# Optimization experiments

Hardware: AMD Instinct MI355X
Metric: run time of the kernel (lower is better)

## Reference

```python
import jax, jax.numpy as jnp
import numpy as np

N_NODES = 50000


def _build_graph(edge_index):
    # Add self-loops (PyG GCNConv default) and compute symmetric normalization.
    n = N_NODES
    loops = jnp.arange(n, dtype=edge_index.dtype)
    src = jnp.concatenate([edge_index[0], loops])
    dst = jnp.concatenate([edge_index[1], loops])
    deg = jax.ops.segment_sum(jnp.ones_like(dst, dtype=jnp.float32), dst, num_segments=n)
    dinv = jax.lax.rsqrt(jnp.maximum(deg, 1e-12))
    norm = dinv[src] * dinv[dst]  # [E+N]
    return src, dst, norm


def _gcn_layer(h, src, dst, norm, W, b):
    # transform-then-propagate: out[dst] += norm * (h @ W)[src]
    h = h @ W  # [N, D_out]
    msg = h[src] * norm[:, None]  # [E+N, D_out]
    agg = jax.ops.segment_sum(msg, dst, num_segments=N_NODES)
    return agg + b


def setup_inputs() -> dict:
    key = jax.random.key(0)
    ks = jax.random.split(key, 8)
    in_dim, hid, out = 128, 64, 32
    n_edges = 800000
    x = jax.random.normal(ks[0], (N_NODES, in_dim), dtype=jnp.float32)
    edge_index = jax.random.randint(ks[1], (2, n_edges), 0, N_NODES, dtype=jnp.int32)
    W1 = jax.random.normal(ks[2], (in_dim, hid), dtype=jnp.float32) / np.sqrt(in_dim)
    b1 = jnp.zeros((hid,), jnp.float32)
    W2 = jax.random.normal(ks[3], (hid, out), dtype=jnp.float32) / np.sqrt(hid)
    b2 = jnp.zeros((out,), jnp.float32)
    attn_w = jax.random.normal(ks[4], (out, 1), dtype=jnp.float32) / np.sqrt(out)
    attn_b = jnp.zeros((1,), jnp.float32)
    return {"x": x, "edge_index": edge_index, "W1": W1, "b1": b1,
            "W2": W2, "b2": b2, "attn_w": attn_w, "attn_b": attn_b}


def reference(x, edge_index, W1, b1, W2, b2, attn_w, attn_b):
    src, dst, norm = _build_graph(edge_index)
    h = jax.nn.relu(_gcn_layer(x, src, dst, norm, W1, b1))
    h = jax.nn.relu(_gcn_layer(h, src, dst, norm, W2, b2))
    attn = jax.nn.sigmoid(h @ attn_w + attn_b)  # [N, 1]
    return h * attn
```

## Files before the change

kernel.cpp:

```cpp
#include <hip/hip_runtime.h>
#include <math.h>

#define N_NODES 50000
#define SLICE_SZ 6250

__global__ void count_kernel(const int* __restrict__ dst, int E, int* __restrict__ counts) {
    int i = blockIdx.x * blockDim.x + threadIdx.x;
    if (i < E) atomicAdd(&counts[dst[i]], 1);
}

__global__ void scan_block_kernel(const int* __restrict__ in, int n,
                                  int* __restrict__ outEx, int* __restrict__ blocksum) {
    __shared__ int s[256];
    int t = threadIdx.x, i = blockIdx.x * 256 + t;
    int v = (i < n) ? in[i] : 0;
    s[t] = v;
    __syncthreads();
    for (int off = 1; off < 256; off <<= 1) {
        int x = (t >= off) ? s[t - off] : 0;
        __syncthreads();
        s[t] += x;
        __syncthreads();
    }
    if (i < n) outEx[i] = s[t] - v;
    if (t == 255 && blocksum) blocksum[blockIdx.x] = s[255];
}

__global__ void finalize_kernel(const int* __restrict__ counts, const int* __restrict__ blocksum,
                                int n, int E, int* __restrict__ row_ptr,
                                int* __restrict__ cursor, float* __restrict__ dinv) {
    int i = blockIdx.x * blockDim.x + threadIdx.x;
    if (i < n) {
        int rp = row_ptr[i] + blocksum[i >> 8];
        row_ptr[i] = rp;
        cursor[i]  = rp;
        dinv[i] = rsqrtf((float)(counts[i] + 1));
        if (i == 0) row_ptr[n] = E;
    }
}

__global__ void fill_sliced_kernel(const int* __restrict__ src, const int* __restrict__ dst,
                                   int E, int* __restrict__ cursor,
                                   const float* __restrict__ dinv, int2* __restrict__ edges) {
    const int slice = blockIdx.x & 7;
    const int chunk = blockIdx.x >> 3;
    const int CS = (E + 255) / 256;
    int lo = chunk * CS;
    int hi = min(E, lo + CS);
    for (int i = lo + threadIdx.x; i < hi; i += 256) {
        int d = dst[i];
        if (d / SLICE_SZ == slice) {
            int s = src[i];
            int p = atomicAdd(&cursor[d], 1);
            edges[p] = make_int2(s, __float_as_int(dinv[s] * dinv[d]));
        }
    }
}

template<int DIN, int DOUT, int BM, int KC>
__global__ __launch_bounds__(256, 2) void gemm_kernel(const float* __restrict__ A,
                                                      const float* __restrict__ W,
                                                      float* __restrict__ C, int n) {
    constexpr int NCG = DOUT / 4;
    constexpr int NRG = BM / 4;
    static_assert(NCG * NRG == 256, "thread mapping");
    constexpr int KG = KC / 4;
    constexpr int RSTEP = 256 / KG;
    __shared__ __align__(16) float ws[DIN * DOUT];
    __shared__ __align__(16) float xs[KC][BM + 4];
    const int t = threadIdx.x;
    for (int i = 4 * t; i < DIN * DOUT; i += 1024)
        *(float4*)&ws[i] = *(const float4*)&W[i];
    const int rowbase = blockIdx.x * BM;
    const int r0 = (t / NCG) * 4;
    const int c0 = (t % NCG) * 4;
    const int lk = (t % KG) * 4;
    const int lr = t / KG;
    float acc[4][4] = {};
    for (int kc = 0; kc < DIN; kc += KC) {
        __syncthreads();
        #pragma unroll
        for (int r = lr; r < BM; r += RSTEP) {
            int row = rowbase + r;
            if (row >= n) row = n - 1;
            float4 v = *(const float4*)&A[(size_t)row * DIN + kc + lk];
            xs[lk + 0][r] = v.x; xs[lk + 1][r] = v.y;
            xs[lk + 2][r] = v.z; xs[lk + 3][r] = v.w;
        }
        __syncthreads();
        #pragma unroll 8
        for (int k = 0; k < KC; ++k) {
            float ar[4], wr[4];
            *(float4*)ar = *(const float4*)&xs[k][r0];
            *(float4*)wr = *(const float4*)&ws[(kc + k) * DOUT + c0];
            #pragma unroll
            for (int i = 0; i < 4; ++i)
                #pragma unroll
                for (int j = 0; j < 4; ++j)
                    acc[i][j] += ar[i] * wr[j];
        }
    }
    #pragma unroll
    for (int i = 0; i < 4; ++i) {
        int row = rowbase + r0 + i;
        if (row < n) {
            float4 v = make_float4(acc[i][0], acc[i][1], acc[i][2], acc[i][3]);
            *(float4*)&C[(size_t)row * DOUT + c0] = v;
        }
    }
}

__global__ __launch_bounds__(256) void gather64_fuse_kernel(
        const float* __restrict__ XW, const int* __restrict__ row_ptr,
        const int2* __restrict__ edges, const float* __restrict__ dinv,
        const float* __restrict__ b1, const float* __restrict__ W2,
        float* __restrict__ out, int n) {
    __shared__ __align__(16) float ws2[64 * 32];
    const int t = threadIdx.x;
    for (int i = 4 * t; i < 64 * 32; i += 1024)
        *(float4*)&ws2[i] = *(const float4*)&W2[i];
    __syncthreads();
    int gid = blockIdx.x * blockDim.x + t;
    int node = gid >> 6;
    int f = t & 63;
    if (node < n) {
        float dv = dinv[node];
        float acc = dv * dv * XW[(size_t)node * 64 + f];
        int e = row_ptr[node], end = row_ptr[node + 1];
        for (; e + 8 <= end; e += 8) {
            int2 p0 = edges[e+0], p1 = edges[e+1], p2 = edges[e+2], p3 = edges[e+3];
            int2 p4 = edges[e+4], p5 = edges[e+5], p6 = edges[e+6], p7 = edges[e+7];
            float v0 = XW[(size_t)p0.x * 64 + f], v1 = XW[(size_t)p1.x * 64 + f];
            float v2 = XW[(size_t)p2.x * 64 + f], v3 = XW[(size_t)p3.x * 64 + f];
            float v4 = XW[(size_t)p4.x * 64 + f], v5 = XW[(size_t)p5.x * 64 + f];
            float v6 = XW[(size_t)p6.x * 64 + f], v7 = XW[(size_t)p7.x * 64 + f];
            acc += __int_as_float(p0.y) * v0; acc += __int_as_float(p1.y) * v1;
            acc += __int_as_float(p2.y) * v2; acc += __int_as_float(p3.y) * v3;
            acc += __int_as_float(p4.y) * v4; acc += __int_as_float(p5.y) * v5;
            acc += __int_as_float(p6.y) * v6; acc += __int_as_float(p7.y) * v7;
        }
        if (e + 4 <= end) {
            int2 p0 = edges[e+0], p1 = edges[e+1], p2 = edges[e+2], p3 = edges[e+3];
            float v0 = XW[(size_t)p0.x * 64 + f], v1 = XW[(size_t)p1.x * 64 + f];
            float v2 = XW[(size_t)p2.x * 64 + f], v3 = XW[(size_t)p3.x * 64 + f];
            acc += __int_as_float(p0.y) * v0; acc += __int_as_float(p1.y) * v1;
            acc += __int_as_float(p2.y) * v2; acc += __int_as_float(p3.y) * v3;
            e += 4;
        }
        for (; e < end; ++e) {
            int2 p = edges[e];
            acc += __int_as_float(p.y) * XW[(size_t)p.x * 64 + f];
        }
        float h = fmaxf(acc + b1[f], 0.f);
        int j = f & 31, half = f >> 5;
        int fbase = half << 5;
        float y = 0.f;
        #pragma unroll
        for (int k = 0; k < 32; ++k) {
            float hf = __shfl(h, fbase + k, 64);
            y += hf * ws2[(fbase + k) * 32 + j];
        }
        y += __shfl_xor(y, 32, 64);
        if (half == 0) out[(size_t)node * 32 + j] = y;
    }
}

__global__ __launch_bounds__(256) void gather32_final_kernel(
        const float* __restrict__ XW, const int* __restrict__ row_ptr,
        const int2* __restrict__ edges, const float* __restrict__ dinv,
        const float* __restrict__ bias, const float* __restrict__ aw,
        const float* __restrict__ ab, float* __restrict__ out, int n) {
    int gid = blockIdx.x * blockDim.x + threadIdx.x;
    int node = gid >> 6;
    int lane = threadIdx.x & 63;
    int f = lane & 31, half = lane >> 5;
    if (node >= n) return;
    float acc = 0.f;
    if (half == 0) {
        float dv = dinv[node];
        acc = dv * dv * XW[(size_t)node * 32 + f];
    }
    int end = row_ptr[node + 1];
    int e = row_ptr[node] + half;
    for (; e + 6 < end; e += 8) {
        int2 p0 = edges[e+0], p1 = edges[e+2], p2 = edges[e+4], p3 = edges[e+6];
        float v0 = XW[(size_t)p0.x * 32 + f], v1 = XW[(size_t)p1.x * 32 + f];
        float v2 = XW[(size_t)p2.x * 32 + f], v3 = XW[(size_t)p3.x * 32 + f];
        acc += __int_as_float(p0.y) * v0; acc += __int_as_float(p1.y) * v1;
        acc += __int_as_float(p2.y) * v2; acc += __int_as_float(p3.y) * v3;
    }
    for (; e < end; e += 2) {
        int2 p = edges[e];
        acc += __int_as_float(p.y) * XW[(size_t)p.x * 32 + f];
    }
    acc += __shfl_xor(acc, 32, 64);
    float h = fmaxf(acc + bias[f], 0.f);
    float sca = h * aw[f];
    #pragma unroll
    for (int m = 16; m >= 1; m >>= 1) sca += __shfl_xor(sca, m, 64);
    float attn = 1.f / (1.f + __expf(-(sca + ab[0])));
    if (half == 0) out[(size_t)node * 32 + f] = h * attn;
}

extern "C" void kernel_launch(void* const* d_in, const int* in_sizes, int n_in,
                              void* d_out, int out_size, void* d_ws, size_t ws_size,
                              hipStream_t stream) {
    const float* x  = (const float*)d_in[0];
    const int*   ei = (const int*)d_in[1];
    const float* W1 = (const float*)d_in[2];
    const float* b1 = (const float*)d_in[3];
    const float* W2 = (const float*)d_in[4];
    const float* b2 = (const float*)d_in[5];
    const float* aw = (const float*)d_in[6];
    const float* ab = (const float*)d_in[7];
    float* out = (float*)d_out;

    const int n = N_NODES;
    const int E = in_sizes[1] / 2;
    const int* src = ei;
    const int* dst = ei + E;

    char* w = (char*)d_ws;
    auto alloc = [&](size_t bytes) { char* p = w; w += (bytes + 255) & ~(size_t)255; return p; };
    int*   counts   = (int*)  alloc((size_t)n * 4);
    int*   row_ptr  = (int*)  alloc((size_t)(n + 1) * 4);
    int*   cursor   = (int*)  alloc((size_t)n * 4);
    int*   blocksum = (int*)  alloc(1024);
    float* dinv     = (float*)alloc((size_t)n * 4);
    int2*  edges    = (int2*) alloc((size_t)E * 8);
    float* bufA     = (float*)alloc((size_t)n * 64 * 4);
    float* bufB     = (float*)alloc((size_t)n * 32 * 4);

    const int nb = (n + 255) / 256;

    hipMemsetAsync(counts, 0, (size_t)n * 4, stream);
    count_kernel<<<(E + 255) / 256, 256, 0, stream>>>(dst, E, counts);
    scan_block_kernel<<<nb, 256, 0, stream>>>(counts, n, row_ptr, blocksum);
    scan_block_kernel<<<1, 256, 0, stream>>>(blocksum, nb, blocksum, nullptr);
    finalize_kernel<<<nb, 256, 0, stream>>>(counts, blocksum, n, E, row_ptr, cursor, dinv);
    fill_sliced_kernel<<<256 * 8, 256, 0, stream>>>(src, dst, E, cursor, dinv, edges);

    gemm_kernel<128, 64, 64, 32><<<(n + 63) / 64, 256, 0, stream>>>(x, W1, bufA, n);
    gather64_fuse_kernel<<<((size_t)n * 64 + 255) / 256, 256, 0, stream>>>(
        bufA, row_ptr, edges, dinv, b1, W2, bufB, n);
    gather32_final_kernel<<<((size_t)n * 64 + 255) / 256, 256, 0, stream>>>(
        bufB, row_ptr, edges, dinv, b2, aw, ab, out, n);
}
```

Before: 263.3 us.

## Precompute edge ranks in count pass and vectorize gathers with float4 multi-way lanes

The count kernel now records each edge's atomic rank, so the fill kernel computes CSR positions as row_ptr plus rank with no second atomic pass. The fill kernel also reads dst as int4. Both gather kernels switch from one-feature-per-lane scalar loads to float4 loads, with several lanes ('ways') splitting each node's edges and combining through shuffle reductions. The layer-2 matvec uses a padded, permuted shared-memory copy of W2. This cuts atomics and memory transactions, at the cost of an extra E-sized rank buffer and more shuffle work.

```diff
diff --git a/kernel.cpp b/kernel.cpp
--- a/kernel.cpp
+++ b/kernel.cpp
@@ -4,9 +4,14 @@
 #define N_NODES 50000
 #define SLICE_SZ 6250
 
-__global__ void count_kernel(const int* __restrict__ dst, int E, int* __restrict__ counts) {
+__device__ __forceinline__ void fma4(float4& a, float w, const float4& v) {
+    a.x += w * v.x; a.y += w * v.y; a.z += w * v.z; a.w += w * v.w;
+}
+
+__global__ void count_kernel(const int* __restrict__ dst, int E,
+                             int* __restrict__ counts, int* __restrict__ rank) {
     int i = blockIdx.x * blockDim.x + threadIdx.x;
-    if (i < E) atomicAdd(&counts[dst[i]], 1);
+    if (i < E) rank[i] = atomicAdd(&counts[dst[i]], 1);
 }
 
 __global__ void scan_block_kernel(const int* __restrict__ in, int n,
@@ -28,30 +33,44 @@
 
 __global__ void finalize_kernel(const int* __restrict__ counts, const int* __restrict__ blocksum,
                                 int n, int E, int* __restrict__ row_ptr,
-                                int* __restrict__ cursor, float* __restrict__ dinv) {
+                                float* __restrict__ dinv) {
     int i = blockIdx.x * blockDim.x + threadIdx.x;
     if (i < n) {
-        int rp = row_ptr[i] + blocksum[i >> 8];
-        row_ptr[i] = rp;
-        cursor[i]  = rp;
+        row_ptr[i] += blocksum[i >> 8];
         dinv[i] = rsqrtf((float)(counts[i] + 1));
         if (i == 0) row_ptr[n] = E;
     }
 }
 
-__global__ void fill_sliced_kernel(const int* __restrict__ src, const int* __restrict__ dst,
-                                   int E, int* __restrict__ cursor,
-                                   const float* __restrict__ dinv, int2* __restrict__ edges) {
+__global__ void fill2_kernel(const int* __restrict__ src, const int* __restrict__ dst,
+                             const int* __restrict__ rank, int E,
+                             const int* __restrict__ row_ptr, const float* __restrict__ dinv,
+                             int2* __restrict__ edges) {
     const int slice = blockIdx.x & 7;
     const int chunk = blockIdx.x >> 3;
-    const int CS = (E + 255) / 256;
-    int lo = chunk * CS;
-    int hi = min(E, lo + CS);
-    for (int i = lo + threadIdx.x; i < hi; i += 256) {
+    const int CS = (((E + 255) >> 8) + 3) & ~3;
+    const int lo = chunk * CS;
+    const int hi = min(E, lo + CS);
+    const int slo = slice * SLICE_SZ, shi = slo + SLICE_SZ;
+    if (lo >= E) return;
+    const int quad_end = lo + ((hi - lo) & ~3);
+    for (int i = lo + threadIdx.x * 4; i + 3 < quad_end + 4 && i + 3 < hi + 4 && i < quad_end; i += 1024) {
+        int4 d4 = *(const int4*)&dst[i];
+        #pragma unroll
+        for (int k = 0; k < 4; ++k) {
+            int d = (&d4.x)[k];
+            if (d >= slo && d < shi) {
+                int s = src[i + k];
+                int p = row_ptr[d] + rank[i + k];
+                edges[p] = make_int2(s, __float_as_int(dinv[s] * dinv[d]));
+            }
+        }
+    }
+    for (int i = quad_end + threadIdx.x; i < hi; i += 256) {
         int d = dst[i];
-        if (d / SLICE_SZ == slice) {
+        if (d >= slo && d < shi) {
             int s = src[i];
-            int p = atomicAdd(&cursor[d], 1);
+            int p = row_ptr[d] + rank[i];
             edges[p] = make_int2(s, __float_as_int(dinv[s] * dinv[d]));
         }
     }
@@ -115,91 +134,128 @@
         const int2* __restrict__ edges, const float* __restrict__ dinv,
         const float* __restrict__ b1, const float* __restrict__ W2,
         float* __restrict__ out, int n) {
-    __shared__ __align__(16) float ws2[64 * 32];
+    __shared__ float ws2R[64 * 33];
     const int t = threadIdx.x;
-    for (int i = 4 * t; i < 64 * 32; i += 1024)
-        *(float4*)&ws2[i] = *(const float4*)&W2[i];
+    for (int i = t; i < 64 * 32; i += 256) {
+        int f = i >> 5, j = i & 31;
+        ws2R[f * 33 + (((j & 7) << 2) | (j >> 3))] = W2[i];
+    }
     __syncthreads();
-    int gid = blockIdx.x * blockDim.x + t;
-    int node = gid >> 6;
-    int f = t & 63;
-    if (node < n) {
+    const int node = blockIdx.x * 4 + (t >> 6);
+    if (node >= n) return;
+    const int lane = t & 63;
+    const int fg = lane & 15, way = lane >> 4;
+    const float4* __restrict__ XW4 = (const float4*)XW;
+    float4 acc = make_float4(0.f, 0.f, 0.f, 0.f);
+    if (way == 0) {
         float dv = dinv[node];
-        float acc = dv * dv * XW[(size_t)node * 64 + f];
-        int e = row_ptr[node], end = row_ptr[node + 1];
-        for (; e + 8 <= end; e += 8) {
-            int2 p0 = edges[e+0], p1 = edges[e+1], p2 = edges[e+2], p3 = edges[e+3];
-            int2 p4 = edges[e+4], p5 = edges[e+5], p6 = edges[e+6], p7 = edges[e+7];
-            float v0 = XW[(size_t)p0.x * 64 + f], v1 = XW[(size_t)p1.x * 64 + f];
-            float v2 = XW[(size_t)p2.x * 64 + f], v3 = XW[(size_t)p3.x * 64 + f];
-            float v4 = XW[(size_t)p4.x * 64 + f], v5 = XW[(size_t)p5.x * 64 + f];
-            float v6 = XW[(size_t)p6.x * 64 + f], v7 = XW[(size_t)p7.x * 64 + f];
-            acc += __int_as_float(p0.y) * v0; acc += __int_as_float(p1.y) * v1;
-            acc += __int_as_float(p2.y) * v2; acc += __int_as_float(p3.y) * v3;
-            acc += __int_as_float(p4.y) * v4; acc += __int_as_float(p5.y) * v5;
-            acc += __int_as_float(p6.y) * v6; acc += __int_as_float(p7.y) * v7;
-        }
-        if (e + 4 <= end) {
-            int2 p0 = edges[e+0], p1 = edges[e+1], p2 = edges[e+2], p3 = edges[e+3];
-            float v0 = XW[(size_t)p0.x * 64 + f], v1 = XW[(size_t)p1.x * 64 + f];
-            float v2 = XW[(size_t)p2.x * 64 + f], v3 = XW[(size_t)p3.x * 64 + f];
-            acc += __int_as_float(p0.y) * v0; acc += __int_as_float(p1.y) * v1;
-            acc += __int_as_float(p2.y) * v2; acc += __int_as_float(p3.y) * v3;
-            e += 4;
-        }
-        for (; e < end; ++e) {
-            int2 p = edges[e];
-            acc += __int_as_float(p.y) * XW[(size_t)p.x * 64 + f];
-        }
-        float h = fmaxf(acc + b1[f], 0.f);
-        int j = f & 31, half = f >> 5;
-        int fbase = half << 5;
-        float y = 0.f;
+        float4 v = XW4[(size_t)node * 16 + fg];
+        float s2 = dv * dv;
+        acc.x = s2 * v.x; acc.y = s2 * v.y; acc.z = s2 * v.z; acc.w = s2 * v.w;
+    }
+    int e = row_ptr[node] + way;
+    const int end = row_ptr[node + 1];
+    for (; e + 4 < end; e += 8) {
+        int2 p0 = edges[e], p1 = edges[e + 4];
+        float4 v0 = XW4[(size_t)p0.x * 16 + fg];
+        float4 v1 = XW4[(size_t)p1.x * 16 + fg];
+        fma4(acc, __int_as_float(p0.y), v0);
+        fma4(acc, __int_as_float(p1.y), v1);
+    }
+    for (; e < end; e += 4) {
+        int2 p = edges[e];
+        float4 v = XW4[(size_t)p.x * 16 + fg];
+        fma4(acc, __int_as_float(p.y), v);
+    }
+    #pragma unroll
+    for (int m = 16; m <= 32; m <<= 1) {
+        acc.x += __shfl_xor(acc.x, m, 64);
+        acc.y += __shfl_xor(acc.y, m, 64);
+        acc.z += __shfl_xor(acc.z, m, 64);
+        acc.w += __shfl_xor(acc.w, m, 64);
+    }
+    float4 b = ((const float4*)b1)[fg];
+    float4 h;
+    h.x = fmaxf(acc.x + b.x, 0.f);
+    h.y = fmaxf(acc.y + b.y, 0.f);
+    h.z = fmaxf(acc.z + b.z, 0.f);
+    h.w = fmaxf(acc.w + b.w, 0.f);
+    const int rbase = fg * 132;
+    float py[8];
+    #pragma unroll
+    for (int s = 0; s < 8; ++s) {
+        int idx = rbase + 4 * s + way;
+        py[s] = h.x * ws2R[idx]
+              + h.y * ws2R[idx + 33]
+              + h.z * ws2R[idx + 66]
+              + h.w * ws2R[idx + 99];
+    }
+    #pragma unroll
+    for (int m = 1; m <= 8; m <<= 1) {
         #pragma unroll
-        for (int k = 0; k < 32; ++k) {
-            float hf = __shfl(h, fbase + k, 64);
-            y += hf * ws2[(fbase + k) * 32 + j];
-        }
-        y += __shfl_xor(y, 32, 64);
-        if (half == 0) out[(size_t)node * 32 + j] = y;
+        for (int s = 0; s < 8; ++s) py[s] += __shfl_xor(py[s], m, 64);
+    }
+    if (fg == 0) {
+        float4* o = (float4*)&out[(size_t)node * 32 + way * 8];
+        o[0] = make_float4(py[0], py[1], py[2], py[3]);
+        o[1] = make_float4(py[4], py[5], py[6], py[7]);
     }
 }
 
 __global__ __launch_bounds__(256) void gather32_final_kernel(
         const float* __restrict__ XW, const int* __restrict__ row_ptr,
         const int2* __restrict__ edges, const float* __restrict__ dinv,
-        const float* __restrict__ bias, const float* __restrict__ aw,
+        const float* __restrict__ b2, const float* __restrict__ aw,
         const float* __restrict__ ab, float* __restrict__ out, int n) {
-    int gid = blockIdx.x * blockDim.x + threadIdx.x;
-    int node = gid >> 6;
-    int lane = threadIdx.x & 63;
-    int f = lane & 31, half = lane >> 5;
+    const int t = threadIdx.x;
+    const int node = blockIdx.x * 4 + (t >> 6);
     if (node >= n) return;
-    float acc = 0.f;
-    if (half == 0) {
+    const int lane = t & 63;
+    const int fg = lane & 7, way = lane >> 3;
+    const float4* __restrict__ XW4 = (const float4*)XW;
+    float4 acc = make_float4(0.f, 0.f, 0.f, 0.f);
+    if (way == 0) {
         float dv = dinv[node];
-        acc = dv * dv * XW[(size_t)node * 32 + f];
-    }
-    int end = row_ptr[node + 1];
-    int e = row_ptr[node] + half;
-    for (; e + 6 < end; e += 8) {
-        int2 p0 = edges[e+0], p1 = edges[e+2], p2 = edges[e+4], p3 = edges[e+6];
-        float v0 = XW[(size_t)p0.x * 32 + f], v1 = XW[(size_t)p1.x * 32 + f];
-        float v2 = XW[(size_t)p2.x * 32 + f], v3 = XW[(size_t)p3.x * 32 + f];
-        acc += __int_as_float(p0.y) * v0; acc += __int_as_float(p1.y) * v1;
-        acc += __int_as_float(p2.y) * v2; acc += __int_as_float(p3.y) * v3;
-    }
-    for (; e < end; e += 2) {
+        float4 v = XW4[(size_t)node * 8 + fg];
+        float s2 = dv * dv;
+        acc.x = s2 * v.x; acc.y = s2 * v.y; acc.z = s2 * v.z; acc.w = s2 * v.w;
+    }
+    int e = row_ptr[node] + way;
+    const int end = row_ptr[node + 1];
+    for (; e + 8 < end; e += 16) {
+        int2 p0 = edges[e], p1 = edges[e + 8];
+        float4 v0 = XW4[(size_t)p0.x * 8 + fg];
+        float4 v1 = XW4[(size_t)p1.x * 8 + fg];
+        fma4(acc, __int_as_float(p0.y), v0);
+        fma4(acc, __int_as_float(p1.y), v1);
+    }
+    for (; e < end; e += 8) {
         int2 p = edges[e];
-        acc += __int_as_float(p.y) * XW[(size_t)p.x * 32 + f];
-    }
-    acc += __shfl_xor(acc, 32, 64);
-    float h = fmaxf(acc + bias[f], 0.f);
-    float sca = h * aw[f];
-    #pragma unroll
-    for (int m = 16; m >= 1; m >>= 1) sca += __shfl_xor(sca, m, 64);
+        fma4(acc, __int_as_float(p.y), XW4[(size_t)p.x * 8 + fg]);
+    }
+    #pragma unroll
+    for (int m = 8; m <= 32; m <<= 1) {
+        acc.x += __shfl_xor(acc.x, m, 64);
+        acc.y += __shfl_xor(acc.y, m, 64);
+        acc.z += __shfl_xor(acc.z, m, 64);
+        acc.w += __shfl_xor(acc.w, m, 64);
+    }
+    float4 b = ((const float4*)b2)[fg];
+    float4 h;
+    h.x = fmaxf(acc.x + b.x, 0.f);
+    h.y = fmaxf(acc.y + b.y, 0.f);
+    h.z = fmaxf(acc.z + b.z, 0.f);
+    h.w = fmaxf(acc.w + b.w, 0.f);
+    float4 a4 = ((const float4*)aw)[fg];
+    float sca = h.x * a4.x + h.y * a4.y + h.z * a4.z + h.w * a4.w;
+    sca += __shfl_xor(sca, 1, 64);
+    sca += __shfl_xor(sca, 2, 64);
+    sca += __shfl_xor(sca, 4, 64);
     float attn = 1.f / (1.f + __expf(-(sca + ab[0])));
-    if (half == 0) out[(size_t)node * 32 + f] = h * attn;
+    if (way == 0) {
+        float4 r = make_float4(h.x * attn, h.y * attn, h.z * attn, h.w * attn);
+        ((float4*)&out[(size_t)node * 32])[fg] = r;
+    }
 }
 
 extern "C" void kernel_launch(void* const* d_in, const int* in_sizes, int n_in,
@@ -224,7 +280,7 @@
     auto alloc = [&](size_t bytes) { char* p = w; w += (bytes + 255) & ~(size_t)255; return p; };
     int*   counts   = (int*)  alloc((size_t)n * 4);
     int*   row_ptr  = (int*)  alloc((size_t)(n + 1) * 4);
-    int*   cursor   = (int*)  alloc((size_t)n * 4);
+    int*   rank     = (int*)  alloc((size_t)E * 4);
     int*   blocksum = (int*)  alloc(1024);
     float* dinv     = (float*)alloc((size_t)n * 4);
     int2*  edges    = (int2*) alloc((size_t)E * 8);
@@ -234,15 +290,15 @@
     const int nb = (n + 255) / 256;
 
     hipMemsetAsync(counts, 0, (size_t)n * 4, stream);
-    count_kernel<<<(E + 255) / 256, 256, 0, stream>>>(dst, E, counts);
+    count_kernel<<<(E + 255) / 256, 256, 0, stream>>>(dst, E, counts, rank);
     scan_block_kernel<<<nb, 256, 0, stream>>>(counts, n, row_ptr, blocksum);
     scan_block_kernel<<<1, 256, 0, stream>>>(blocksum, nb, blocksum, nullptr);
-    finalize_kernel<<<nb, 256, 0, stream>>>(counts, blocksum, n, E, row_ptr, cursor, dinv);
-    fill_sliced_kernel<<<256 * 8, 256, 0, stream>>>(src, dst, E, cursor, dinv, edges);
+    finalize_kernel<<<nb, 256, 0, stream>>>(counts, blocksum, n, E, row_ptr, dinv);
+    fill2_kernel<<<256 * 8, 256, 0, stream>>>(src, dst, rank, E, row_ptr, dinv, edges);
 
     gemm_kernel<128, 64, 64, 32><<<(n + 63) / 64, 256, 0, stream>>>(x, W1, bufA, n);
-    gather64_fuse_kernel<<<((size_t)n * 64 + 255) / 256, 256, 0, stream>>>(
+    gather64_fuse_kernel<<<(n + 3) / 4, 256, 0, stream>>>(
         bufA, row_ptr, edges, dinv, b1, W2, bufB, n);
-    gather32_final_kernel<<<((size_t)n * 64 + 255) / 256, 256, 0, stream>>>(
+    gather32_final_kernel<<<(n + 3) / 4, 256, 0, stream>>>(
         bufB, row_ptr, edges, dinv, b2, aw, ab, out, n);
 }
```

After: 250.3 us. 1.05x faster.
